# Performance work log

Measured on AMD Instinct MI355X. Metric: run time of the kernel, lower is better.

## Reference

```python
import jax, jax.numpy as jnp
import numpy as np

DIM = 1024
SEGMENT_SIZE = 1024
DILATION_RATE = 2

def setup_inputs() -> dict:
    key = jax.random.key(0)
    x = jax.random.normal(key, (4, 8192, DIM), dtype=jnp.float32)
    return {"x": x}

def reference(x) -> jnp.ndarray:
    B, S, D = x.shape
    pad = (-S) % SEGMENT_SIZE
    x = jnp.pad(x, ((0, 0), (0, pad), (0, 0)))
    # [B, n_seg, segment_size, D]
    x = x.reshape(B, -1, SEGMENT_SIZE, D)
    # dilation: strided slice within each segment -> [B, n_seg, seg', D]
    x = x[:, :, ::DILATION_RATE, :]
    q = k = v = x
    scale = 1.0 / jnp.sqrt(jnp.asarray(D, dtype=x.dtype))
    # attention within each segment over dilated tokens (non-causal, no dropout)
    scores = jnp.einsum('bsqd,bskd->bsqk', q, k) * scale
    probs = jax.nn.softmax(scores, axis=-1)
    attn = jnp.einsum('bsqk,bskd->bsqd', probs, v)
    # flatten segments back to a (shortened, dilated) sequence
    return attn.reshape(B, -1, D)
```

## Files before the change

### kernel.cpp

```cpp
#include <hip/hip_runtime.h>


typedef float          f32x4  __attribute__((ext_vector_type(4)));
typedef short          bf16x8 __attribute__((ext_vector_type(8)));
typedef unsigned short u16x8  __attribute__((ext_vector_type(8)));

#define MFMA16(a, b, c) __builtin_amdgcn_mfma_f32_16x16x32_bf16((a), (b), (c), 0, 0, 0)

static __device__ __forceinline__ unsigned short f2bf(float f) {
    unsigned u = __float_as_uint(f);
    u = (u + 0x7fffu + ((u >> 16) & 1u)) >> 16;
    return (unsigned short)u;
}
static __device__ __forceinline__ float bf2f(unsigned short h) {
    return __uint_as_float(((unsigned)h) << 16);
}

static __device__ __forceinline__ void async_cp16(const unsigned short* g, unsigned short* l) {
    __builtin_amdgcn_global_load_lds((const __attribute__((address_space(1))) unsigned int*)g,
                                     (__attribute__((address_space(3))) unsigned int*)l,
                                     16, 0, 0);
}

static __device__ __forceinline__ void stage_tile(const unsigned short* __restrict__ src,
                                                  unsigned short* lds,
                                                  int row_stride, int col0,
                                                  int wave, int lane) {
    const int pr = lane >> 3;
    const int lc = (lane & 7) ^ pr;
    #pragma unroll
    for (int c = 0; c < 4; ++c) {
        const int chunk = wave * 4 + c;
        async_cp16(src + (size_t)(chunk * 8 + pr) * row_stride + col0 + lc * 8,
                   lds + chunk * 512);
    }
}

__global__ __launch_bounds__(256) void k_prep(const float* __restrict__ x,
                                              unsigned short* __restrict__ Xb,
                                              unsigned short* __restrict__ VT) {
    const int kb = blockIdx.x, db = blockIdx.y, g = blockIdx.z;
    const int t = threadIdx.x;
    __shared__ unsigned short Ts[64][72];
    {
        const int r = t >> 2, q = t & 3;
        const float* src = x + ((size_t)g << 20) + (size_t)(kb * 64 + r) * 2048 + db * 64 + q * 16;
        alignas(16) unsigned short tmp[16];
        #pragma unroll
        for (int i = 0; i < 4; ++i) {
            const float4 v = *reinterpret_cast<const float4*>(src + i * 4);
            tmp[i * 4 + 0] = f2bf(v.x); tmp[i * 4 + 1] = f2bf(v.y);
            tmp[i * 4 + 2] = f2bf(v.z); tmp[i * 4 + 3] = f2bf(v.w);
        }
        unsigned short* xb = Xb + ((size_t)g * 512 + kb * 64 + r) * 1024 + db * 64 + q * 16;
        *reinterpret_cast<uint4*>(xb)     = *reinterpret_cast<const uint4*>(&tmp[0]);
        *reinterpret_cast<uint4*>(xb + 8) = *reinterpret_cast<const uint4*>(&tmp[8]);
        *reinterpret_cast<uint4*>(&Ts[r][q * 16])     = *reinterpret_cast<const uint4*>(&tmp[0]);
        *reinterpret_cast<uint4*>(&Ts[r][q * 16 + 8]) = *reinterpret_cast<const uint4*>(&tmp[8]);
    }
    __syncthreads();
    {
        const int dl = t >> 2, kq = t & 3;
        alignas(16) unsigned short o[16];
        #pragma unroll
        for (int j = 0; j < 16; ++j) o[j] = Ts[kq * 16 + j][dl];
        unsigned short* vt = VT + ((size_t)g * 1024 + db * 64 + dl) * 512 + kb * 64 + kq * 16;
        *reinterpret_cast<uint4*>(vt)     = *reinterpret_cast<const uint4*>(&o[0]);
        *reinterpret_cast<uint4*>(vt + 8) = *reinterpret_cast<const uint4*>(&o[8]);
    }
}

__global__ __launch_bounds__(256) void k_scores(const unsigned short* __restrict__ Xb,
                                                unsigned short* __restrict__ S) {
    const int nb = blockIdx.x, mb = blockIdx.y, g = blockIdx.z;
    const int tid = threadIdx.x, wave = tid >> 6, lane = tid & 63;
    const int g4 = lane >> 4, n16 = lane & 15;
    const int wr = wave & 1, wc = wave >> 1;

    __shared__ unsigned short As[128 * 64];
    __shared__ unsigned short Bs[128 * 64];

    const unsigned short* Ag = Xb + ((size_t)g * 512 + mb * 128) * 1024;
    const unsigned short* Bg = Xb + ((size_t)g * 512 + nb * 128) * 1024;

    f32x4 acc[16];
    const f32x4 vzero = {0.f, 0.f, 0.f, 0.f};
    #pragma unroll
    for (int i = 0; i < 16; ++i) acc[i] = vzero;

    for (int kt = 0; kt < 16; ++kt) {
        if (kt) __syncthreads();
        stage_tile(Ag, As, 1024, kt * 64, wave, lane);
        stage_tile(Bg, Bs, 1024, kt * 64, wave, lane);
        __syncthreads();
        #pragma unroll
        for (int ks = 0; ks < 2; ++ks) {
            const int sw = ((ks * 4 + g4) ^ (n16 & 7)) * 8;
            bf16x8 a[4], b[4];
            #pragma unroll
            for (int i = 0; i < 4; ++i)
                a[i] = *reinterpret_cast<const bf16x8*>(&As[(wr * 64 + i * 16 + n16) * 64 + sw]);
            #pragma unroll
            for (int j = 0; j < 4; ++j)
                b[j] = *reinterpret_cast<const bf16x8*>(&Bs[(wc * 64 + j * 16 + n16) * 64 + sw]);
            #pragma unroll
            for (int i = 0; i < 4; ++i)
                #pragma unroll
                for (int j = 0; j < 4; ++j)
                    acc[i * 4 + j] = MFMA16(a[i], b[j], acc[i * 4 + j]);
        }
    }

    unsigned short* Sg = S + ((size_t)g * 512 + mb * 128 + wr * 64) * 512 + nb * 128 + wc * 64;
    #pragma unroll
    for (int i = 0; i < 4; ++i)
        #pragma unroll
        for (int j = 0; j < 4; ++j)
            #pragma unroll
            for (int r = 0; r < 4; ++r)
                Sg[(size_t)(i * 16 + g4 * 4 + r) * 512 + j * 16 + n16] =
                    f2bf(acc[i * 4 + j][r] * 0.03125f);
}

__global__ __launch_bounds__(256) void k_softmax(unsigned short* __restrict__ S) {
    const int wave = threadIdx.x >> 6, lane = threadIdx.x & 63;
    unsigned short* row = S + ((size_t)blockIdx.x * 4 + wave) * 512;

    u16x8 v = *reinterpret_cast<const u16x8*>(row + lane * 8);
    float f[8];
    #pragma unroll
    for (int k = 0; k < 8; ++k) f[k] = bf2f(v[k]);

    float m = f[0];
    #pragma unroll
    for (int k = 1; k < 8; ++k) m = fmaxf(m, f[k]);
    #pragma unroll
    for (int d = 1; d < 64; d <<= 1) m = fmaxf(m, __shfl_xor(m, d, 64));

    float s = 0.f;
    #pragma unroll
    for (int k = 0; k < 8; ++k) { f[k] = __expf(f[k] - m); s += f[k]; }
    #pragma unroll
    for (int d = 1; d < 64; d <<= 1) s += __shfl_xor(s, d, 64);
    const float inv = 1.0f / s;

    u16x8 o;
    #pragma unroll
    for (int k = 0; k < 8; ++k) o[k] = f2bf(f[k] * inv);
    *reinterpret_cast<u16x8*>(row + lane * 8) = o;
}

__global__ __launch_bounds__(256) void k_pv(const unsigned short* __restrict__ P,
                                            const unsigned short* __restrict__ VT,
                                            float* __restrict__ out) {
    const int nb = blockIdx.x, mb = blockIdx.y, g = blockIdx.z;
    const int tid = threadIdx.x, wave = tid >> 6, lane = tid & 63;
    const int g4 = lane >> 4, n16 = lane & 15;
    const int wr = wave & 1, wc = wave >> 1;

    __shared__ unsigned short As[128 * 64];
    __shared__ unsigned short Bs[128 * 64];

    const unsigned short* Ag = P  + ((size_t)g * 512  + mb * 128) * 512;
    const unsigned short* Bg = VT + ((size_t)g * 1024 + nb * 128) * 512;

    f32x4 acc[16];
    const f32x4 vzero = {0.f, 0.f, 0.f, 0.f};
    #pragma unroll
    for (int i = 0; i < 16; ++i) acc[i] = vzero;

    for (int kt = 0; kt < 8; ++kt) {
        if (kt) __syncthreads();
        stage_tile(Ag, As, 512, kt * 64, wave, lane);
        stage_tile(Bg, Bs, 512, kt * 64, wave, lane);
        __syncthreads();
        #pragma unroll
        for (int ks = 0; ks < 2; ++ks) {
            const int sw = ((ks * 4 + g4) ^ (n16 & 7)) * 8;
            bf16x8 a[4], b[4];
            #pragma unroll
            for (int i = 0; i < 4; ++i)
                a[i] = *reinterpret_cast<const bf16x8*>(&As[(wr * 64 + i * 16 + n16) * 64 + sw]);
            #pragma unroll
            for (int j = 0; j < 4; ++j)
                b[j] = *reinterpret_cast<const bf16x8*>(&Bs[(wc * 64 + j * 16 + n16) * 64 + sw]);
            #pragma unroll
            for (int i = 0; i < 4; ++i)
                #pragma unroll
                for (int j = 0; j < 4; ++j)
                    acc[i * 4 + j] = MFMA16(a[i], b[j], acc[i * 4 + j]);
        }
    }

    float* og = out + ((size_t)g * 512 + mb * 128 + wr * 64) * 1024 + nb * 128 + wc * 64;
    #pragma unroll
    for (int i = 0; i < 4; ++i)
        #pragma unroll
        for (int j = 0; j < 4; ++j)
            #pragma unroll
            for (int r = 0; r < 4; ++r)
                og[(size_t)(i * 16 + g4 * 4 + r) * 1024 + j * 16 + n16] = acc[i * 4 + j][r];
}

extern "C" void kernel_launch(void* const* d_in, const int* in_sizes, int n_in,
                              void* d_out, int out_size, void* d_ws, size_t ws_size,
                              hipStream_t stream) {
    const float* x = (const float*)d_in[0];
    float* out = (float*)d_out;

    unsigned short* S  = (unsigned short*)d_ws;
    unsigned short* Xb = S  + (size_t)32 * 512 * 512;
    unsigned short* VT = Xb + (size_t)32 * 512 * 1024;

    k_prep   <<<dim3(8, 16, 32), 256, 0, stream>>>(x, Xb, VT);
    k_scores <<<dim3(4, 4, 32),  256, 0, stream>>>(Xb, S);
    k_softmax<<<4096,            256, 0, stream>>>(S);
    k_pv     <<<dim3(8, 4, 32),  256, 0, stream>>>(S, VT, out);
}
```

Before: 258.5 us.

## Fuse softmax into score and PV kernels using unnormalized exp and atomic row sums

Drops the separate softmax kernel. The scores kernel now writes exp(score) directly, without subtracting the row max, and atomically adds partial row sums into a workspace buffer. The PV kernel divides its output by those sums in the epilogue. The grid order is also changed so the group index varies fastest. This saves one read/write pass over the score matrix and one launch, but it adds a memset, atomics, and a risk of overflow if the scores are large.

```diff
diff --git a/kernel.cpp b/kernel.cpp
--- a/kernel.cpp
+++ b/kernel.cpp
@@ -3,7 +3,6 @@
 
 typedef float          f32x4  __attribute__((ext_vector_type(4)));
 typedef short          bf16x8 __attribute__((ext_vector_type(8)));
-typedef unsigned short u16x8  __attribute__((ext_vector_type(8)));
 
 #define MFMA16(a, b, c) __builtin_amdgcn_mfma_f32_16x16x32_bf16((a), (b), (c), 0, 0, 0)
 
@@ -11,9 +10,6 @@
     unsigned u = __float_as_uint(f);
     u = (u + 0x7fffu + ((u >> 16) & 1u)) >> 16;
     return (unsigned short)u;
-}
-static __device__ __forceinline__ float bf2f(unsigned short h) {
-    return __uint_as_float(((unsigned)h) << 16);
 }
 
 static __device__ __forceinline__ void async_cp16(const unsigned short* g, unsigned short* l) {
@@ -71,14 +67,16 @@
 }
 
 __global__ __launch_bounds__(256) void k_scores(const unsigned short* __restrict__ Xb,
-                                                unsigned short* __restrict__ S) {
-    const int nb = blockIdx.x, mb = blockIdx.y, g = blockIdx.z;
+                                                unsigned short* __restrict__ T,
+                                                float* __restrict__ Lsum) {
+    const int g = blockIdx.x, nb = blockIdx.y, mb = blockIdx.z;
     const int tid = threadIdx.x, wave = tid >> 6, lane = tid & 63;
     const int g4 = lane >> 4, n16 = lane & 15;
     const int wr = wave & 1, wc = wave >> 1;
 
     __shared__ unsigned short As[128 * 64];
     __shared__ unsigned short Bs[128 * 64];
+    __shared__ float red[4][64];
 
     const unsigned short* Ag = Xb + ((size_t)g * 512 + mb * 128) * 1024;
     const unsigned short* Bg = Xb + ((size_t)g * 512 + nb * 128) * 1024;
@@ -111,57 +109,62 @@
         }
     }
 
-    unsigned short* Sg = S + ((size_t)g * 512 + mb * 128 + wr * 64) * 512 + nb * 128 + wc * 64;
+    float rs[4][4];
+    #pragma unroll
+    for (int i = 0; i < 4; ++i)
+        #pragma unroll
+        for (int r = 0; r < 4; ++r) rs[i][r] = 0.f;
+
+    unsigned short* Tg = T + ((size_t)g * 512 + mb * 128 + wr * 64) * 512 + nb * 128 + wc * 64;
     #pragma unroll
     for (int i = 0; i < 4; ++i)
         #pragma unroll
         for (int j = 0; j < 4; ++j)
             #pragma unroll
+            for (int r = 0; r < 4; ++r) {
+                const float e = __expf(acc[i * 4 + j][r] * 0.03125f);
+                rs[i][r] += e;
+                Tg[(size_t)(i * 16 + g4 * 4 + r) * 512 + j * 16 + n16] = f2bf(e);
+            }
+
+    #pragma unroll
+    for (int d = 1; d < 16; d <<= 1)
+        #pragma unroll
+        for (int i = 0; i < 4; ++i)
+            #pragma unroll
             for (int r = 0; r < 4; ++r)
-                Sg[(size_t)(i * 16 + g4 * 4 + r) * 512 + j * 16 + n16] =
-                    f2bf(acc[i * 4 + j][r] * 0.03125f);
-}
-
-__global__ __launch_bounds__(256) void k_softmax(unsigned short* __restrict__ S) {
-    const int wave = threadIdx.x >> 6, lane = threadIdx.x & 63;
-    unsigned short* row = S + ((size_t)blockIdx.x * 4 + wave) * 512;
-
-    u16x8 v = *reinterpret_cast<const u16x8*>(row + lane * 8);
-    float f[8];
-    #pragma unroll
-    for (int k = 0; k < 8; ++k) f[k] = bf2f(v[k]);
-
-    float m = f[0];
-    #pragma unroll
-    for (int k = 1; k < 8; ++k) m = fmaxf(m, f[k]);
-    #pragma unroll
-    for (int d = 1; d < 64; d <<= 1) m = fmaxf(m, __shfl_xor(m, d, 64));
-
-    float s = 0.f;
-    #pragma unroll
-    for (int k = 0; k < 8; ++k) { f[k] = __expf(f[k] - m); s += f[k]; }
-    #pragma unroll
-    for (int d = 1; d < 64; d <<= 1) s += __shfl_xor(s, d, 64);
-    const float inv = 1.0f / s;
-
-    u16x8 o;
-    #pragma unroll
-    for (int k = 0; k < 8; ++k) o[k] = f2bf(f[k] * inv);
-    *reinterpret_cast<u16x8*>(row + lane * 8) = o;
-}
-
-__global__ __launch_bounds__(256) void k_pv(const unsigned short* __restrict__ P,
+                rs[i][r] += __shfl_xor(rs[i][r], d, 64);
+    if (n16 == 0) {
+        #pragma unroll
+        for (int i = 0; i < 4; ++i)
+            #pragma unroll
+            for (int r = 0; r < 4; ++r)
+                red[wave][i * 16 + g4 * 4 + r] = rs[i][r];
+    }
+    __syncthreads();
+    if (tid < 128) {
+        const int h = tid >> 6, idx = tid & 63;
+        atomicAdd(&Lsum[g * 512 + mb * 128 + h * 64 + idx],
+                  red[h][idx] + red[h + 2][idx]);
+    }
+}
+
+__global__ __launch_bounds__(256) void k_pv(const unsigned short* __restrict__ T,
                                             const unsigned short* __restrict__ VT,
+                                            const float* __restrict__ Lsum,
                                             float* __restrict__ out) {
-    const int nb = blockIdx.x, mb = blockIdx.y, g = blockIdx.z;
+    const int g = blockIdx.x, nb = blockIdx.y, mb = blockIdx.z;
     const int tid = threadIdx.x, wave = tid >> 6, lane = tid & 63;
     const int g4 = lane >> 4, n16 = lane & 15;
     const int wr = wave & 1, wc = wave >> 1;
 
     __shared__ unsigned short As[128 * 64];
     __shared__ unsigned short Bs[128 * 64];
-
-    const unsigned short* Ag = P  + ((size_t)g * 512  + mb * 128) * 512;
+    __shared__ float Linv[128];
+
+    if (tid < 128) Linv[tid] = 1.0f / Lsum[g * 512 + mb * 128 + tid];
+
+    const unsigned short* Ag = T  + ((size_t)g * 512  + mb * 128) * 512;
     const unsigned short* Bg = VT + ((size_t)g * 1024 + nb * 128) * 512;
 
     f32x4 acc[16];
@@ -170,7 +173,7 @@
     for (int i = 0; i < 16; ++i) acc[i] = vzero;
 
     for (int kt = 0; kt < 8; ++kt) {
-        if (kt) __syncthreads();
+        __syncthreads();
         stage_tile(Ag, As, 512, kt * 64, wave, lane);
         stage_tile(Bg, Bs, 512, kt * 64, wave, lane);
         __syncthreads();
@@ -192,6 +195,13 @@
         }
     }
 
+    float li[4][4];
+    #pragma unroll
+    for (int i = 0; i < 4; ++i)
+        #pragma unroll
+        for (int r = 0; r < 4; ++r)
+            li[i][r] = Linv[wr * 64 + i * 16 + g4 * 4 + r];
+
     float* og = out + ((size_t)g * 512 + mb * 128 + wr * 64) * 1024 + nb * 128 + wc * 64;
     #pragma unroll
     for (int i = 0; i < 4; ++i)
@@ -199,7 +209,8 @@
         for (int j = 0; j < 4; ++j)
             #pragma unroll
             for (int r = 0; r < 4; ++r)
-                og[(size_t)(i * 16 + g4 * 4 + r) * 1024 + j * 16 + n16] = acc[i * 4 + j][r];
+                og[(size_t)(i * 16 + g4 * 4 + r) * 1024 + j * 16 + n16] =
+                    acc[i * 4 + j][r] * li[i][r];
 }
 
 extern "C" void kernel_launch(void* const* d_in, const int* in_sizes, int n_in,
@@ -208,12 +219,13 @@
     const float* x = (const float*)d_in[0];
     float* out = (float*)d_out;
 
-    unsigned short* S  = (unsigned short*)d_ws;
-    unsigned short* Xb = S  + (size_t)32 * 512 * 512;
+    unsigned short* T  = (unsigned short*)d_ws;
+    unsigned short* Xb = T  + (size_t)32 * 512 * 512;
     unsigned short* VT = Xb + (size_t)32 * 512 * 1024;
-
-    k_prep   <<<dim3(8, 16, 32), 256, 0, stream>>>(x, Xb, VT);
-    k_scores <<<dim3(4, 4, 32),  256, 0, stream>>>(Xb, S);
-    k_softmax<<<4096,            256, 0, stream>>>(S);
-    k_pv     <<<dim3(8, 4, 32),  256, 0, stream>>>(S, VT, out);
-}
+    float*          Ls = (float*)(VT + (size_t)32 * 1024 * 512);
+
+    hipMemsetAsync(Ls, 0, 32 * 512 * sizeof(float), stream);
+    k_prep  <<<dim3(8, 16, 32), 256, 0, stream>>>(x, Xb, VT);
+    k_scores<<<dim3(32, 4, 4),  256, 0, stream>>>(Xb, T, Ls);
+    k_pv    <<<dim3(32, 8, 4),  256, 0, stream>>>(T, VT, Ls, out);
+}
```

New measurement: 247.5 us. -4.3%, faster.
